# Kernel optimization log

Hardware: AMD Instinct MI355X
Metric: run time of the kernel (lower is better)

The kernel has to match this reference:

```python
import jax, jax.numpy as jnp
import numpy as np

COLOR_SIZE = 4
SIZE = 128
LENGTH = SIZE * SIZE * 3  # 49152


def setup_inputs() -> dict:
    key = jax.random.key(0)
    k1, k2, k3, k4 = jax.random.split(key, 4)
    example = jax.random.randint(k1, (2, SIZE, SIZE, 3), 0, COLOR_SIZE, dtype=jnp.int32)
    W_in = jax.random.normal(k2, (1, 1024), dtype=jnp.float32) * 0.02
    pos_enc = jax.random.normal(k3, (LENGTH, 1024), dtype=jnp.float32)
    W_final = jax.random.normal(k4, (1024, COLOR_SIZE), dtype=jnp.float32) * 0.02
    b_final = jnp.zeros((COLOR_SIZE,), dtype=jnp.float32)
    return {"example": example, "W_in": W_in, "pos_enc": pos_enc,
            "W_final": W_final, "b_final": b_final}


def reference(example, W_in, pos_enc, W_final, b_final):
    # example: [B, 128, 128, 3] int, values in [0, color_size)
    B = example.shape[0]
    x = example.astype(jnp.float32) / COLOR_SIZE * 2.0 - 1.0
    x = x.reshape(B, LENGTH, 1)
    x = x * 2.0 - 1.0  # second scaling, as in original call()
    x = x @ W_in  # [B, L, 1] @ [1, F] -> [B, L, F]
    x = jax.nn.relu(x + pos_enc)
    # running-average via causal cumsum; factor computed in fp16 as in original
    factor = (1.0 / jnp.arange(1, LENGTH + 1, dtype=jnp.float32))
    factor = factor.astype(jnp.float16).astype(jnp.float32)[:, None]
    x = jnp.cumsum(x, axis=-2) * factor
    x = x @ W_final + b_final  # [B, L, color_size]
    x = x.reshape(B, SIZE, SIZE, 3, COLOR_SIZE)
    return x.astype(jnp.float32)
```

## Files before the change

kernel.cpp:

```cpp
#include <hip/hip_runtime.h>
#include <math.h>

#define L_TOTAL 49152
#define NBLK 768
#define ROWS_PER_BLK 64
#define ROWS_PER_WAVE 16
#define NWGROUPS (NBLK * 4)
#define SCR_STRIDE 520

__device__ __forceinline__ float4 f4add(float4 a, float4 b) {
  return make_float4(a.x + b.x, a.y + b.y, a.z + b.z, a.w + b.w);
}

__device__ __forceinline__ float fp16_roundtrip_pos(float x) {
  unsigned u = __float_as_uint(x);
  int e = (int)((u >> 23) & 0xffu) - 127;
  unsigned m = (u & 0x7fffffu) | 0x800000u;
  int shift = (e >= -14) ? 13 : (13 + (-14 - e));
  if (shift >= 25) return 0.0f;
  unsigned keep = m >> shift;
  unsigned rem = m & ((1u << shift) - 1u);
  unsigned halfbit = 1u << (shift - 1);
  if (rem > halfbit || (rem == halfbit && (keep & 1u))) keep++;
  return ldexpf((float)keep, e + shift - 23);
}

__global__ __launch_bounds__(256, 3) void gpart_kernel(
    const int* __restrict__ ex, const float4* __restrict__ win4,
    const float4* __restrict__ pos4, const float4* __restrict__ wf4,
    float* __restrict__ gf, float* __restrict__ ppwf) {
  __shared__ float scratch[4][4 * SCR_STRIDE];

  const int lane = threadIdx.x & 63;
  const int wv = threadIdx.x >> 6;
  float* scr = scratch[wv];
  const int rowBase = blockIdx.x * ROWS_PER_BLK + wv * ROWS_PER_WAVE;

  float4 win[4];
  float4 wf[4][4];
#pragma unroll
  for (int j = 0; j < 4; ++j) {
    const int fi = j * 64 + lane;
    win[j] = win4[fi];
#pragma unroll
    for (int k = 0; k < 4; ++k) wf[j][k] = wf4[fi * 4 + k];
  }

  const int rhat = lane >> 4;
  const int chat = (lane >> 1) & 7;
  const int h = lane & 1;

  float carry = 0.0f;

  for (int batch = 0; batch < 4; ++batch) {
#pragma unroll
    for (int r = 0; r < 4; ++r) {
      const int l = rowBase + batch * 4 + r;
      const float s0 = (float)ex[l] - 3.0f;
      const float s1 = (float)ex[L_TOTAL + l] - 3.0f;
      float4 a0 = make_float4(0.f, 0.f, 0.f, 0.f);
      float4 a1 = make_float4(0.f, 0.f, 0.f, 0.f);
#pragma unroll
      for (int j = 0; j < 4; ++j) {
        const float4 p = pos4[(size_t)l * 256 + j * 64 + lane];
        const float pc[4] = {p.x, p.y, p.z, p.w};
        const float wc[4] = {win[j].x, win[j].y, win[j].z, win[j].w};
#pragma unroll
        for (int k = 0; k < 4; ++k) {
          const float t0 = fmaxf(fmaf(s0, wc[k], pc[k]), 0.0f);
          const float t1 = fmaxf(fmaf(s1, wc[k], pc[k]), 0.0f);
          const float4 w = wf[j][k];
          a0.x = fmaf(t0, w.x, a0.x); a0.y = fmaf(t0, w.y, a0.y);
          a0.z = fmaf(t0, w.z, a0.z); a0.w = fmaf(t0, w.w, a0.w);
          a1.x = fmaf(t1, w.x, a1.x); a1.y = fmaf(t1, w.y, a1.y);
          a1.z = fmaf(t1, w.z, a1.z); a1.w = fmaf(t1, w.w, a1.w);
        }
      }
      float* dst = &scr[r * SCR_STRIDE + lane * 8];
      *(float4*)(dst) = a0;
      *(float4*)(dst + 4) = a1;
    }

    const float* src = &scr[rhat * SCR_STRIDE + h * 32 * 8 + chat];
    float s = 0.0f;
#pragma unroll
    for (int i = 0; i < 32; ++i) s += src[i * 8];
    s += __shfl_xor(s, 1);

    {
      float u = __shfl_up(s, 16);
      if (rhat >= 1) s += u;
      u = __shfl_up(s, 32);
      if (rhat >= 2) s += u;
    }
    const float vout = s + carry;
    carry = __shfl(vout, 48 + (lane & 15));

    if (h == 0) {
      const int row = rowBase + batch * 4 + rhat;
      gf[(size_t)(chat >> 2) * L_TOTAL * 4 + (size_t)row * 4 + (chat & 3)] =
          vout;
    }
  }

  if (h == 0 && rhat == 0) {
    const int wg = blockIdx.x * 4 + wv;
    ppwf[(size_t)(chat >> 2) * NWGROUPS * 4 + (size_t)wg * 4 + (chat & 3)] =
        carry;
  }
}

__global__ __launch_bounds__(128, 8) void finish_kernel(
    const float4* __restrict__ g4, const float4* __restrict__ ppw,
    const float* __restrict__ bfin, float4* __restrict__ out4) {
  const int tid = threadIdx.x;
  const int bb = tid >> 6;
  const int i = tid & 63;
  const int bid = blockIdx.x;
  const int wgBase = bid * 4;

  float4 q = make_float4(0.f, 0.f, 0.f, 0.f);
  for (int j = i; j < wgBase; j += 64) q = f4add(q, ppw[bb * NWGROUPS + j]);
#pragma unroll
  for (int off = 32; off > 0; off >>= 1) {
    q.x += __shfl_xor(q.x, off); q.y += __shfl_xor(q.y, off);
    q.z += __shfl_xor(q.z, off); q.w += __shfl_xor(q.w, off);
  }
  const int gsub = i >> 4;
  for (int k = 0; k < gsub; ++k)
    q = f4add(q, ppw[bb * NWGROUPS + wgBase + k]);

  const int row = bid * ROWS_PER_BLK + i;
  const float4 v = f4add(g4[(size_t)bb * L_TOTAL + row], q);
  const float factor = fp16_roundtrip_pos(1.0f / (float)(row + 1));
  float4 o;
  o.x = fmaf(v.x, factor, bfin[0]);
  o.y = fmaf(v.y, factor, bfin[1]);
  o.z = fmaf(v.z, factor, bfin[2]);
  o.w = fmaf(v.w, factor, bfin[3]);
  out4[(size_t)bb * L_TOTAL + row] = o;
}

extern "C" void kernel_launch(void* const* d_in, const int* in_sizes, int n_in,
                              void* d_out, int out_size, void* d_ws, size_t ws_size,
                              hipStream_t stream) {
  const int* ex = (const int*)d_in[0];
  const float4* win4 = (const float4*)d_in[1];
  const float4* pos4 = (const float4*)d_in[2];
  const float4* wf4 = (const float4*)d_in[3];
  const float* bfin = (const float*)d_in[4];
  float4* out4 = (float4*)d_out;

  float* gf = (float*)d_ws;
  float* ppwf = gf + (size_t)2 * L_TOTAL * 4;

  gpart_kernel<<<NBLK, 256, 0, stream>>>(ex, win4, pos4, wf4, gf, ppwf);
  finish_kernel<<<NBLK, 128, 0, stream>>>((const float4*)gf,
                                          (const float4*)ppwf, bfin, out4);
}
```

Before: 54.85 us.

## Map each lane to a row with LDS-staged pos_enc tiles and register scans

The main kernel now assigns one row per 16-lane segment. Each 64-row block streams pos_enc through a double-buffered shared-memory tile, 32 features per chunk, instead of each wave splitting the features of a single row across its lanes. The per-row 4-wide products are reduced across segments with shuffles, and the row prefix sum is done with shuffle scans plus a cross-wave shared-memory step. This removes the per-row LDS scratch reduction and writes one carry per block instead of one per wave. The trade-off is a __syncthreads per chunk and per-chunk global loads of W_in and W_final from cache, where they were previously held in registers.

```diff
diff --git a/kernel.cpp b/kernel.cpp
--- a/kernel.cpp
+++ b/kernel.cpp
@@ -4,9 +4,7 @@
 #define L_TOTAL 49152
 #define NBLK 768
 #define ROWS_PER_BLK 64
-#define ROWS_PER_WAVE 16
-#define NWGROUPS (NBLK * 4)
-#define SCR_STRIDE 520
+#define NCHUNK 32
 
 __device__ __forceinline__ float4 f4add(float4 a, float4 b) {
   return make_float4(a.x + b.x, a.y + b.y, a.z + b.z, a.w + b.w);
@@ -28,110 +26,126 @@
 __global__ __launch_bounds__(256, 3) void gpart_kernel(
     const int* __restrict__ ex, const float4* __restrict__ win4,
     const float4* __restrict__ pos4, const float4* __restrict__ wf4,
-    float* __restrict__ gf, float* __restrict__ ppwf) {
-  __shared__ float scratch[4][4 * SCR_STRIDE];
+    float4* __restrict__ gbuf, float4* __restrict__ pp) {
+  __shared__ float4 tile[2][ROWS_PER_BLK][9];
+  __shared__ float4 wtot[2][4];
 
-  const int lane = threadIdx.x & 63;
-  const int wv = threadIdx.x >> 6;
-  float* scr = scratch[wv];
-  const int rowBase = blockIdx.x * ROWS_PER_BLK + wv * ROWS_PER_WAVE;
+  const int tid = threadIdx.x;
+  const int lane = tid & 63;
+  const int wv = tid >> 6;
+  const int rowBase = blockIdx.x * ROWS_PER_BLK;
 
-  float4 win[4];
-  float4 wf[4][4];
+  const int r_st = tid >> 2;
+  const int q_st = tid & 3;
+
+  const int seg = lane >> 4;
+  const int r16 = lane & 15;
+  const int myrow = wv * 16 + r16;
+  const int grow = rowBase + myrow;
+
+  const float s0 = (float)ex[grow] - 3.0f;
+  const float s1 = (float)ex[L_TOTAL + grow] - 3.0f;
+
+  float4 a0 = make_float4(0.f, 0.f, 0.f, 0.f);
+  float4 a1 = make_float4(0.f, 0.f, 0.f, 0.f);
+
+  const size_t prow = (size_t)(rowBase + r_st) * 256;
+
+  tile[0][r_st][q_st]     = pos4[prow + q_st];
+  tile[0][r_st][q_st + 4] = pos4[prow + q_st + 4];
+  __syncthreads();
+
+  for (int c = 0; c < NCHUNK; ++c) {
+    if (c + 1 < NCHUNK) {
+      const int f4n = (c + 1) * 8;
+      tile[(c + 1) & 1][r_st][q_st]     = pos4[prow + f4n + q_st];
+      tile[(c + 1) & 1][r_st][q_st + 4] = pos4[prow + f4n + q_st + 4];
+    }
+    const int f4b = c * 8 + seg * 2;
+    const float4 p0 = tile[c & 1][myrow][seg * 2];
+    const float4 p1 = tile[c & 1][myrow][seg * 2 + 1];
+    const float4 w0 = win4[f4b];
+    const float4 w1 = win4[f4b + 1];
+    const float pe[8] = {p0.x, p0.y, p0.z, p0.w, p1.x, p1.y, p1.z, p1.w};
+    const float we[8] = {w0.x, w0.y, w0.z, w0.w, w1.x, w1.y, w1.z, w1.w};
 #pragma unroll
-  for (int j = 0; j < 4; ++j) {
-    const int fi = j * 64 + lane;
-    win[j] = win4[fi];
-#pragma unroll
-    for (int k = 0; k < 4; ++k) wf[j][k] = wf4[fi * 4 + k];
+    for (int e = 0; e < 8; ++e) {
+      const float4 wf = wf4[f4b * 4 + e];
+      const float t0 = fmaxf(fmaf(s0, we[e], pe[e]), 0.0f);
+      const float t1 = fmaxf(fmaf(s1, we[e], pe[e]), 0.0f);
+      a0.x = fmaf(t0, wf.x, a0.x); a0.y = fmaf(t0, wf.y, a0.y);
+      a0.z = fmaf(t0, wf.z, a0.z); a0.w = fmaf(t0, wf.w, a0.w);
+      a1.x = fmaf(t1, wf.x, a1.x); a1.y = fmaf(t1, wf.y, a1.y);
+      a1.z = fmaf(t1, wf.z, a1.z); a1.w = fmaf(t1, wf.w, a1.w);
+    }
+    __syncthreads();
   }
 
-  const int rhat = lane >> 4;
-  const int chat = (lane >> 1) & 7;
-  const int h = lane & 1;
+#define REDUCE8(MASK)                                                   \
+  a0.x += __shfl_xor(a0.x, MASK); a0.y += __shfl_xor(a0.y, MASK);       \
+  a0.z += __shfl_xor(a0.z, MASK); a0.w += __shfl_xor(a0.w, MASK);       \
+  a1.x += __shfl_xor(a1.x, MASK); a1.y += __shfl_xor(a1.y, MASK);       \
+  a1.z += __shfl_xor(a1.z, MASK); a1.w += __shfl_xor(a1.w, MASK);
+  REDUCE8(16)
+  REDUCE8(32)
+#undef REDUCE8
 
-  float carry = 0.0f;
-
-  for (int batch = 0; batch < 4; ++batch) {
 #pragma unroll
-    for (int r = 0; r < 4; ++r) {
-      const int l = rowBase + batch * 4 + r;
-      const float s0 = (float)ex[l] - 3.0f;
-      const float s1 = (float)ex[L_TOTAL + l] - 3.0f;
-      float4 a0 = make_float4(0.f, 0.f, 0.f, 0.f);
-      float4 a1 = make_float4(0.f, 0.f, 0.f, 0.f);
-#pragma unroll
-      for (int j = 0; j < 4; ++j) {
-        const float4 p = pos4[(size_t)l * 256 + j * 64 + lane];
-        const float pc[4] = {p.x, p.y, p.z, p.w};
-        const float wc[4] = {win[j].x, win[j].y, win[j].z, win[j].w};
-#pragma unroll
-        for (int k = 0; k < 4; ++k) {
-          const float t0 = fmaxf(fmaf(s0, wc[k], pc[k]), 0.0f);
-          const float t1 = fmaxf(fmaf(s1, wc[k], pc[k]), 0.0f);
-          const float4 w = wf[j][k];
-          a0.x = fmaf(t0, w.x, a0.x); a0.y = fmaf(t0, w.y, a0.y);
-          a0.z = fmaf(t0, w.z, a0.z); a0.w = fmaf(t0, w.w, a0.w);
-          a1.x = fmaf(t1, w.x, a1.x); a1.y = fmaf(t1, w.y, a1.y);
-          a1.z = fmaf(t1, w.z, a1.z); a1.w = fmaf(t1, w.w, a1.w);
-        }
-      }
-      float* dst = &scr[r * SCR_STRIDE + lane * 8];
-      *(float4*)(dst) = a0;
-      *(float4*)(dst + 4) = a1;
-    }
-
-    const float* src = &scr[rhat * SCR_STRIDE + h * 32 * 8 + chat];
-    float s = 0.0f;
-#pragma unroll
-    for (int i = 0; i < 32; ++i) s += src[i * 8];
-    s += __shfl_xor(s, 1);
-
-    {
-      float u = __shfl_up(s, 16);
-      if (rhat >= 1) s += u;
-      u = __shfl_up(s, 32);
-      if (rhat >= 2) s += u;
-    }
-    const float vout = s + carry;
-    carry = __shfl(vout, 48 + (lane & 15));
-
-    if (h == 0) {
-      const int row = rowBase + batch * 4 + rhat;
-      gf[(size_t)(chat >> 2) * L_TOTAL * 4 + (size_t)row * 4 + (chat & 3)] =
-          vout;
+  for (int d = 1; d < 16; d <<= 1) {
+    const float u0 = __shfl_up(a0.x, d), u1 = __shfl_up(a0.y, d);
+    const float u2 = __shfl_up(a0.z, d), u3 = __shfl_up(a0.w, d);
+    const float u4 = __shfl_up(a1.x, d), u5 = __shfl_up(a1.y, d);
+    const float u6 = __shfl_up(a1.z, d), u7 = __shfl_up(a1.w, d);
+    if (r16 >= d) {
+      a0.x += u0; a0.y += u1; a0.z += u2; a0.w += u3;
+      a1.x += u4; a1.y += u5; a1.z += u6; a1.w += u7;
     }
   }
 
-  if (h == 0 && rhat == 0) {
-    const int wg = blockIdx.x * 4 + wv;
-    ppwf[(size_t)(chat >> 2) * NWGROUPS * 4 + (size_t)wg * 4 + (chat & 3)] =
-        carry;
+  float4 t0, t1;
+  t0.x = __shfl(a0.x, 15); t0.y = __shfl(a0.y, 15);
+  t0.z = __shfl(a0.z, 15); t0.w = __shfl(a0.w, 15);
+  t1.x = __shfl(a1.x, 15); t1.y = __shfl(a1.y, 15);
+  t1.z = __shfl(a1.z, 15); t1.w = __shfl(a1.w, 15);
+  if (lane == 0) { wtot[0][wv] = t0; wtot[1][wv] = t1; }
+  __syncthreads();
+  float4 o0 = make_float4(0.f, 0.f, 0.f, 0.f);
+  float4 o1 = make_float4(0.f, 0.f, 0.f, 0.f);
+  for (int j = 0; j < wv; ++j) {
+    o0 = f4add(o0, wtot[0][j]);
+    o1 = f4add(o1, wtot[1][j]);
+  }
+  a0 = f4add(a0, o0);
+  a1 = f4add(a1, o1);
+
+  if (seg == 0) {
+    gbuf[grow] = a0;
+    gbuf[L_TOTAL + grow] = a1;
+  }
+  if (tid == 255) {
+    pp[blockIdx.x] = a0;
+    pp[NBLK + blockIdx.x] = a1;
   }
 }
 
 __global__ __launch_bounds__(128, 8) void finish_kernel(
-    const float4* __restrict__ g4, const float4* __restrict__ ppw,
+    const float4* __restrict__ gbuf, const float4* __restrict__ pp,
     const float* __restrict__ bfin, float4* __restrict__ out4) {
   const int tid = threadIdx.x;
   const int bb = tid >> 6;
   const int i = tid & 63;
   const int bid = blockIdx.x;
-  const int wgBase = bid * 4;
 
   float4 q = make_float4(0.f, 0.f, 0.f, 0.f);
-  for (int j = i; j < wgBase; j += 64) q = f4add(q, ppw[bb * NWGROUPS + j]);
+  for (int j = i; j < bid; j += 64) q = f4add(q, pp[bb * NBLK + j]);
 #pragma unroll
   for (int off = 32; off > 0; off >>= 1) {
     q.x += __shfl_xor(q.x, off); q.y += __shfl_xor(q.y, off);
     q.z += __shfl_xor(q.z, off); q.w += __shfl_xor(q.w, off);
   }
-  const int gsub = i >> 4;
-  for (int k = 0; k < gsub; ++k)
-    q = f4add(q, ppw[bb * NWGROUPS + wgBase + k]);
 
   const int row = bid * ROWS_PER_BLK + i;
-  const float4 v = f4add(g4[(size_t)bb * L_TOTAL + row], q);
+  const float4 v = f4add(gbuf[(size_t)bb * L_TOTAL + row], q);
   const float factor = fp16_roundtrip_pos(1.0f / (float)(row + 1));
   float4 o;
   o.x = fmaf(v.x, factor, bfin[0]);
@@ -151,10 +165,9 @@
   const float* bfin = (const float*)d_in[4];
   float4* out4 = (float4*)d_out;
 
-  float* gf = (float*)d_ws;
-  float* ppwf = gf + (size_t)2 * L_TOTAL * 4;
+  float4* gbuf = (float4*)d_ws;
+  float4* pp = gbuf + (size_t)2 * L_TOTAL;
 
-  gpart_kernel<<<NBLK, 256, 0, stream>>>(ex, win4, pos4, wf4, gf, ppwf);
-  finish_kernel<<<NBLK, 128, 0, stream>>>((const float4*)gf,
-                                          (const float4*)ppwf, bfin, out4);
+  gpart_kernel<<<NBLK, 256, 0, stream>>>(ex, win4, pos4, wf4, gbuf, pp);
+  finish_kernel<<<NBLK, 128, 0, stream>>>(gbuf, pp, bfin, out4);
 }
```

Result: faster. 48.77 us (-11.1%).
